# Kernel tuning notes

Hardware: AMD Instinct MI355X
Metric: run time of the kernel (lower is better)

The kernel has to match this reference:

```python
import jax, jax.numpy as jnp
import numpy as np

ALPHA = 1.0  # Student-t degrees of freedom (module default)


def setup_inputs() -> dict:
    key = jax.random.key(0)
    k1, k2 = jax.random.split(key)
    N, D, K = 65536, 512, 256
    x = jax.random.normal(k1, (N, D), dtype=jnp.float32)
    clusters = jax.random.normal(k2, (K, D), dtype=jnp.float32)
    return {"x": x, "clusters": clusters}


def reference(x, clusters):
    # Squared Euclidean distance via norm expansion + GEMM (same math as
    # sum((x[:,None,:] - clusters[None,:,:])**2, axis=2); original then takes
    # sqrt and immediately re-squares, so we use sqdist directly).
    x_sq = jnp.sum(x * x, axis=1, keepdims=True)            # [N,1]
    c_sq = jnp.sum(clusters * clusters, axis=1)             # [K]
    sqdist = x_sq + c_sq[None, :] - 2.0 * (x @ clusters.T)  # [N,K]
    sqdist = jnp.maximum(sqdist, 0.0)
    # Student's t kernel: q_ij = (1 + d^2/alpha)^(-(alpha+1)/2)
    q = (1.0 + sqdist / ALPHA) ** (-(ALPHA + 1.0) / 2.0)
    # Row-normalize to soft assignments
    return q / jnp.sum(q, axis=1, keepdims=True)
```

## Files before the change

### kernel.cpp

```cpp
#include <hip/hip_runtime.h>
#include <hip/hip_bf16.h>
#include <stdint.h>

typedef unsigned short u16;
typedef __attribute__((ext_vector_type(8))) short short8_t;
typedef __attribute__((ext_vector_type(4))) float f32x4;

#define D_DIM 512
#define K_CL  256
#define BM    64
#define NITER 16

__device__ __forceinline__ u16 f2bf(float f) {
  union { float f; uint32_t u; } v; v.f = f;
  uint32_t r = v.u + 0x7fffu + ((v.u >> 16) & 1u);
  return (u16)(r >> 16);
}

__global__ void prep_kernel(const float* __restrict__ clusters,
                            u16* __restrict__ cb, float* __restrict__ csq) {
  int k = blockIdx.x;
  int t = threadIdx.x;
  float4 f = ((const float4*)(clusters + (size_t)k * D_DIM))[t];
  ushort4 u;
  u.x = f2bf(f.x); u.y = f2bf(f.y); u.z = f2bf(f.z); u.w = f2bf(f.w);
  ((ushort4*)(cb + (size_t)k * D_DIM))[t] = u;
  float s = f.x*f.x + f.y*f.y + f.z*f.z + f.w*f.w;
  #pragma unroll
  for (int m = 1; m < 64; m <<= 1) s += __shfl_xor(s, m, 64);
  __shared__ float part[2];
  if ((t & 63) == 0) part[t >> 6] = s;
  __syncthreads();
  if (t == 0) csq[k] = part[0] + part[1];
}

__global__ __launch_bounds__(256, 4)
void cluster_kernel(const float* __restrict__ x,
                    const u16* __restrict__ cb,
                    const float* __restrict__ csq,
                    float* __restrict__ out) {
  __shared__ u16  lA[BM * 32];
  __shared__ u16  lB[K_CL * 32];
  __shared__ float xsq_lds[BM];
  __shared__ float csq_lds[K_CL];
  __shared__ float rowsum[4 * BM];

  const int tid  = threadIdx.x;
  const int lane = tid & 63;
  const int w    = tid >> 6;
  const int quad = lane >> 4;
  const int l16  = lane & 15;
  const int row0 = blockIdx.x * BM;

  csq_lds[tid] = csq[tid];

  const int ar  = tid >> 2;
  const int jga = tid & 3;
  const float* xg = x + (size_t)(row0 + ar) * D_DIM + jga * 8;
  short8_t* aw = (short8_t*)&lA[ar * 32 + jga * 8];

  const u16* bsrc0 = cb + (size_t)ar * D_DIM + jga * 8;

  f32x4 acc[4][4];
  #pragma unroll
  for (int i = 0; i < 4; ++i)
    #pragma unroll
    for (int j = 0; j < 4; ++j)
      acc[i][j] = (f32x4){0.f, 0.f, 0.f, 0.f};

  float sq = 0.f;

  float4 f0 = *(const float4*)(xg);
  float4 f1 = *(const float4*)(xg + 4);

  #pragma unroll 1
  for (int k = 0; k < NITER; ++k) {
    const int kk = k * 32;

    #pragma unroll
    for (int i = 0; i < 4; ++i)
      __builtin_amdgcn_global_load_lds(
          (const __attribute__((address_space(1))) void*)(bsrc0 + i * (64 * D_DIM) + kk),
          (__attribute__((address_space(3))) void*)((char*)lB + (i * 256 + tid) * 16),
          16, 0, 0);

    {
      sq += f0.x*f0.x + f0.y*f0.y + f0.z*f0.z + f0.w*f0.w
          + f1.x*f1.x + f1.y*f1.y + f1.z*f1.z + f1.w*f1.w;
      union { u16 u[8]; short8_t v; } pk;
      pk.u[0]=f2bf(f0.x); pk.u[1]=f2bf(f0.y); pk.u[2]=f2bf(f0.z); pk.u[3]=f2bf(f0.w);
      pk.u[4]=f2bf(f1.x); pk.u[5]=f2bf(f1.y); pk.u[6]=f2bf(f1.z); pk.u[7]=f2bf(f1.w);
      *aw = pk.v;
    }

    if (k < NITER - 1) {
      f0 = *(const float4*)(xg + kk + 32);
      f1 = *(const float4*)(xg + kk + 36);
    }

    __syncthreads();

    short8_t aF[4];
    #pragma unroll
    for (int mi = 0; mi < 4; ++mi)
      aF[mi] = *(const short8_t*)&lA[(mi * 16 + l16) * 32 + quad * 8];
    #pragma unroll
    for (int ni = 0; ni < 4; ++ni) {
      short8_t bF = *(const short8_t*)&lB[(w * 64 + ni * 16 + l16) * 32 + quad * 8];
      #pragma unroll
      for (int mi = 0; mi < 4; ++mi)
        acc[mi][ni] = __builtin_amdgcn_mfma_f32_16x16x32_bf16(
            aF[mi], bF, acc[mi][ni], 0, 0, 0);
    }

    if (k < NITER - 1) __syncthreads();
  }

  sq += __shfl_xor(sq, 1, 64);
  sq += __shfl_xor(sq, 2, 64);
  if ((tid & 3) == 0) xsq_lds[ar] = sq;
  __syncthreads();

  #pragma unroll
  for (int mi = 0; mi < 4; ++mi) {
    #pragma unroll
    for (int v = 0; v < 4; ++v) {
      int row = mi * 16 + quad * 4 + v;
      float xs = xsq_lds[row];
      float s = 0.f;
      #pragma unroll
      for (int ni = 0; ni < 4; ++ni) {
        float d = xs + csq_lds[w * 64 + ni * 16 + l16] - 2.0f * acc[mi][ni][v];
        d = fmaxf(d, 0.f);
        float q = 1.0f / (1.0f + d);
        acc[mi][ni][v] = q;
        s += q;
      }
      s += __shfl_xor(s, 1, 64);
      s += __shfl_xor(s, 2, 64);
      s += __shfl_xor(s, 4, 64);
      s += __shfl_xor(s, 8, 64);
      if (l16 == 0) rowsum[w * 64 + row] = s;
    }
  }
  __syncthreads();

  #pragma unroll
  for (int mi = 0; mi < 4; ++mi) {
    #pragma unroll
    for (int v = 0; v < 4; ++v) {
      int row = mi * 16 + quad * 4 + v;
      float tot = rowsum[row] + rowsum[64 + row] + rowsum[128 + row] + rowsum[192 + row];
      float inv = 1.0f / tot;
      float* orow = out + (size_t)(row0 + row) * K_CL;
      #pragma unroll
      for (int ni = 0; ni < 4; ++ni)
        __builtin_nontemporal_store(acc[mi][ni][v] * inv,
                                    orow + w * 64 + ni * 16 + l16);
    }
  }
}

extern "C" void kernel_launch(void* const* d_in, const int* in_sizes, int n_in,
                              void* d_out, int out_size, void* d_ws, size_t ws_size,
                              hipStream_t stream) {
  const float* x        = (const float*)d_in[0];
  const float* clusters = (const float*)d_in[1];
  float* out = (float*)d_out;
  const int N = in_sizes[0] / D_DIM;

  u16*   cb  = (u16*)d_ws;
  float* csq = (float*)((char*)d_ws + (size_t)K_CL * D_DIM * sizeof(u16));

  prep_kernel<<<K_CL, 128, 0, stream>>>(clusters, cb, csq);
  cluster_kernel<<<N / BM, 256, 0, stream>>>(x, cb, csq, out);
}
```

Measured before the change: 232.3 us.

## Preload full bf16 X tile into swizzled LDS and halve row tile

Row tile drops from 64 to 32, so the grid doubles, and each block now converts its whole 32x512 X slab to bf16 into LDS before the K loop. The old code loaded and converted X one k-chunk at a time inside the loop. LDS layouts for A and B use an XOR swizzle to reduce bank conflicts, and B fragments are loaded before the MFMA batch. This removes per-iteration X global loads from the critical path, but it re-reads the cluster matrix twice as often across blocks and lowers occupancy to 3 blocks per SM because of the larger LDS footprint.

Result: slower. 243.6 us (+4.9%).

```diff
diff --git a/kernel.cpp b/kernel.cpp
--- a/kernel.cpp
+++ b/kernel.cpp
@@ -8,7 +8,7 @@
 
 #define D_DIM 512
 #define K_CL  256
-#define BM    64
+#define BM    32
 #define NITER 16
 
 __device__ __forceinline__ u16 f2bf(float f) {
@@ -34,15 +34,15 @@
   if (t == 0) csq[k] = part[0] + part[1];
 }
 
-__global__ __launch_bounds__(256, 4)
+__global__ __launch_bounds__(256, 3)
 void cluster_kernel(const float* __restrict__ x,
                     const u16* __restrict__ cb,
                     const float* __restrict__ csq,
                     float* __restrict__ out) {
-  __shared__ u16  lA[BM * 32];
-  __shared__ u16  lB[K_CL * 32];
+  __shared__ __align__(16) char lA[BM * D_DIM * 2];
+  __shared__ __align__(16) char lB[K_CL * 32 * 2];
+  __shared__ float csq_lds[K_CL];
   __shared__ float xsq_lds[BM];
-  __shared__ float csq_lds[K_CL];
   __shared__ float rowsum[4 * BM];
 
   const int tid  = threadIdx.x;
@@ -54,83 +54,97 @@
 
   csq_lds[tid] = csq[tid];
 
-  const int ar  = tid >> 2;
-  const int jga = tid & 3;
-  const float* xg = x + (size_t)(row0 + ar) * D_DIM + jga * 8;
-  short8_t* aw = (short8_t*)&lA[ar * 32 + jga * 8];
-
-  const u16* bsrc0 = cb + (size_t)ar * D_DIM + jga * 8;
-
-  f32x4 acc[4][4];
-  #pragma unroll
-  for (int i = 0; i < 4; ++i)
-    #pragma unroll
-    for (int j = 0; j < 4; ++j)
-      acc[i][j] = (f32x4){0.f, 0.f, 0.f, 0.f};
+  const int ar = tid >> 3;
+  const int jc = tid & 7;
+  const float* xg = x + (size_t)(row0 + ar) * D_DIM + jc * 8;
+  const int slab0 = jc >> 2;
+  const int cA = (jc & 3) ^ ((ar >> 1) & 3);
+  char* awbase = lA + ar * 64 + cA * 16;
 
   float sq = 0.f;
-
-  float4 f0 = *(const float4*)(xg);
-  float4 f1 = *(const float4*)(xg + 4);
-
-  #pragma unroll 1
-  for (int k = 0; k < NITER; ++k) {
-    const int kk = k * 32;
-
+  #pragma unroll
+  for (int g = 0; g < 2; ++g) {
+    float4 f[4][2];
     #pragma unroll
-    for (int i = 0; i < 4; ++i)
-      __builtin_amdgcn_global_load_lds(
-          (const __attribute__((address_space(1))) void*)(bsrc0 + i * (64 * D_DIM) + kk),
-          (__attribute__((address_space(3))) void*)((char*)lB + (i * 256 + tid) * 16),
-          16, 0, 0);
-
-    {
+    for (int s4 = 0; s4 < 4; ++s4) {
+      const int s = g * 4 + s4;
+      f[s4][0] = *(const float4*)(xg + s * 64);
+      f[s4][1] = *(const float4*)(xg + s * 64 + 4);
+    }
+    #pragma unroll
+    for (int s4 = 0; s4 < 4; ++s4) {
+      const int s = g * 4 + s4;
+      float4 f0 = f[s4][0], f1 = f[s4][1];
       sq += f0.x*f0.x + f0.y*f0.y + f0.z*f0.z + f0.w*f0.w
           + f1.x*f1.x + f1.y*f1.y + f1.z*f1.z + f1.w*f1.w;
       union { u16 u[8]; short8_t v; } pk;
       pk.u[0]=f2bf(f0.x); pk.u[1]=f2bf(f0.y); pk.u[2]=f2bf(f0.z); pk.u[3]=f2bf(f0.w);
       pk.u[4]=f2bf(f1.x); pk.u[5]=f2bf(f1.y); pk.u[6]=f2bf(f1.z); pk.u[7]=f2bf(f1.w);
-      *aw = pk.v;
+      *(short8_t*)(awbase + (2 * s + slab0) * 2048) = pk.v;
     }
+  }
+  sq += __shfl_xor(sq, 1, 64);
+  sq += __shfl_xor(sq, 2, 64);
+  sq += __shfl_xor(sq, 4, 64);
+  if (jc == 0) xsq_lds[ar] = sq;
 
-    if (k < NITER - 1) {
-      f0 = *(const float4*)(xg + kk + 32);
-      f1 = *(const float4*)(xg + kk + 36);
-    }
+  const int tr = tid >> 2;
+  const int cB = (tid & 3) ^ ((tid >> 3) & 3);
+  const u16* bsrc0 = cb + (size_t)tr * D_DIM + cB * 8;
 
+  f32x4 acc[2][4];
+  #pragma unroll
+  for (int i = 0; i < 2; ++i)
+    #pragma unroll
+    for (int j = 0; j < 4; ++j)
+      acc[i][j] = (f32x4){0.f, 0.f, 0.f, 0.f};
+
+  __syncthreads();
+
+  const int fsw = (quad ^ ((l16 >> 1) & 3)) * 16;
+
+  #pragma unroll 1
+  for (int k16 = 0; k16 < NITER; ++k16) {
+    const int kk = k16 * 32;
+    #pragma unroll
+    for (int i = 0; i < 4; ++i)
+      __builtin_amdgcn_global_load_lds(
+          (const __attribute__((address_space(1))) void*)(bsrc0 + i * (64 * D_DIM) + kk),
+          (__attribute__((address_space(3))) void*)(lB + (i * 256 + tid) * 16),
+          16, 0, 0);
     __syncthreads();
 
-    short8_t aF[4];
+    short8_t aF[2], bF[4];
     #pragma unroll
-    for (int mi = 0; mi < 4; ++mi)
-      aF[mi] = *(const short8_t*)&lA[(mi * 16 + l16) * 32 + quad * 8];
+    for (int mi = 0; mi < 2; ++mi)
+      aF[mi] = *(const short8_t*)(lA + k16 * 2048 + (mi * 16 + l16) * 64 + fsw);
     #pragma unroll
-    for (int ni = 0; ni < 4; ++ni) {
-      short8_t bF = *(const short8_t*)&lB[(w * 64 + ni * 16 + l16) * 32 + quad * 8];
+    for (int ni = 0; ni < 4; ++ni)
+      bF[ni] = *(const short8_t*)(lB + (w * 64 + ni * 16 + l16) * 64 + fsw);
+    #pragma unroll
+    for (int ni = 0; ni < 4; ++ni)
       #pragma unroll
-      for (int mi = 0; mi < 4; ++mi)
+      for (int mi = 0; mi < 2; ++mi)
         acc[mi][ni] = __builtin_amdgcn_mfma_f32_16x16x32_bf16(
-            aF[mi], bF, acc[mi][ni], 0, 0, 0);
-    }
+            aF[mi], bF[ni], acc[mi][ni], 0, 0, 0);
 
-    if (k < NITER - 1) __syncthreads();
+    if (k16 < NITER - 1) __syncthreads();
   }
 
-  sq += __shfl_xor(sq, 1, 64);
-  sq += __shfl_xor(sq, 2, 64);
-  if ((tid & 3) == 0) xsq_lds[ar] = sq;
-  __syncthreads();
+  float cs[4];
+  #pragma unroll
+  for (int ni = 0; ni < 4; ++ni) cs[ni] = csq_lds[w * 64 + ni * 16 + l16];
 
   #pragma unroll
-  for (int mi = 0; mi < 4; ++mi) {
+  for (int mi = 0; mi < 2; ++mi) {
     #pragma unroll
     for (int v = 0; v < 4; ++v) {
-      int row = mi * 16 + quad * 4 + v;
-      float xs = xsq_lds[row];
+      const int row = mi * 16 + quad * 4 + v;
+      const float xs = xsq_lds[row];
       float s = 0.f;
       #pragma unroll
       for (int ni = 0; ni < 4; ++ni) {
-        float d = xs + csq_lds[w * 64 + ni * 16 + l16] - 2.0f * acc[mi][ni][v];
+        float d = xs + cs[ni] - 2.0f * acc[mi][ni][v];
         d = fmaxf(d, 0.f);
         float q = 1.0f / (1.0f + d);
         acc[mi][ni][v] = q;
@@ -140,18 +154,19 @@
       s += __shfl_xor(s, 2, 64);
       s += __shfl_xor(s, 4, 64);
       s += __shfl_xor(s, 8, 64);
-      if (l16 == 0) rowsum[w * 64 + row] = s;
+      if (l16 == 0) rowsum[w * BM + row] = s;
     }
   }
   __syncthreads();
 
   #pragma unroll
-  for (int mi = 0; mi < 4; ++mi) {
+  for (int mi = 0; mi < 2; ++mi) {
     #pragma unroll
     for (int v = 0; v < 4; ++v) {
-      int row = mi * 16 + quad * 4 + v;
-      float tot = rowsum[row] + rowsum[64 + row] + rowsum[128 + row] + rowsum[192 + row];
-      float inv = 1.0f / tot;
+      const int row = mi * 16 + quad * 4 + v;
+      const float tot = rowsum[row] + rowsum[BM + row]
+                      + rowsum[2 * BM + row] + rowsum[3 * BM + row];
+      const float inv = 1.0f / tot;
       float* orow = out + (size_t)(row0 + row) * K_CL;
       #pragma unroll
       for (int ni = 0; ni < 4; ++ni)
```
